# Kernel optimization log

Hardware: AMD Instinct MI355X
Metric: run time of the kernel (lower is better)

The kernel has to match this reference:

```python
import jax, jax.numpy as jnp
import numpy as np

BN_EPS = 1e-5
NUM_GRAPHS = 64


def setup_inputs() -> dict:
    key = jax.random.key(0)
    ks = jax.random.split(key, 10)
    N, F, H, E = 50000, 128, 256, 800000
    x = jax.random.normal(ks[0], (N, F), dtype=jnp.float32)
    edge_index = jax.random.randint(ks[1], (2, E), 0, N, dtype=jnp.int64)
    batch = jnp.sort(jax.random.randint(ks[2], (N,), 0, NUM_GRAPHS, dtype=jnp.int64))
    # Linear weights stored as [in, out]; y = z @ w + b (equivalent to torch Linear)
    w1_0 = jax.random.normal(ks[3], (F, H), dtype=jnp.float32) / np.sqrt(F)
    b1_0 = jnp.zeros((H,), jnp.float32)
    w2_0 = jax.random.normal(ks[4], (H, H), dtype=jnp.float32) / np.sqrt(H)
    b2_0 = jnp.zeros((H,), jnp.float32)
    g_0 = jnp.ones((H,), jnp.float32)
    be_0 = jnp.zeros((H,), jnp.float32)
    w1_r = jax.random.normal(ks[5], (3, H, H), dtype=jnp.float32) / np.sqrt(H)
    b1_r = jnp.zeros((3, H), jnp.float32)
    w2_r = jax.random.normal(ks[6], (3, H, H), dtype=jnp.float32) / np.sqrt(H)
    b2_r = jnp.zeros((3, H), jnp.float32)
    g_r = jnp.ones((3, H), jnp.float32)
    be_r = jnp.zeros((3, H), jnp.float32)
    return dict(x=x, edge_index=edge_index, batch=batch,
                w1_0=w1_0, b1_0=b1_0, w2_0=w2_0, b2_0=b2_0, g_0=g_0, be_0=be_0,
                w1_r=w1_r, b1_r=b1_r, w2_r=w2_r, b2_r=b2_r, g_r=g_r, be_r=be_r)


def _gin_layer(h, src, dst, n, w1, b1, w2, b2, g, be):
    # GINConv with eps=0: MLP(h_i + sum_{j->i} h_j), scatter-add over edges
    agg = jax.ops.segment_sum(h[src], dst, num_segments=n)  # [N, d]
    z = agg + h
    z = jnp.maximum(z @ w1 + b1, 0.0)
    z = z @ w2 + b2
    # BatchNorm1d over the node dimension (training-mode batch statistics)
    mu = jnp.mean(z, axis=0)
    var = jnp.var(z, axis=0)
    z = (z - mu) * jax.lax.rsqrt(var + BN_EPS) * g + be
    return jnp.maximum(z, 0.0)  # ReLU; dropout is identity in eval mode


def reference(x, edge_index, batch, w1_0, b1_0, w2_0, b2_0, g_0, be_0,
              w1_r, b1_r, w2_r, b2_r, g_r, be_r):
    src, dst = edge_index[0], edge_index[1]
    n = x.shape[0]
    h = _gin_layer(x, src, dst, n, w1_0, b1_0, w2_0, b2_0, g_0, be_0)
    for i in range(3):
        h = _gin_layer(h, src, dst, n, w1_r[i], b1_r[i], w2_r[i], b2_r[i], g_r[i], be_r[i])
    # global mean pool per graph id
    counts = jax.ops.segment_sum(jnp.ones((n,), h.dtype), batch, num_segments=NUM_GRAPHS)
    pooled = jax.ops.segment_sum(h, batch, num_segments=NUM_GRAPHS)
    return pooled / jnp.maximum(counts, 1.0)[:, None]
```

## Files before the change

### kernel.cpp

```cpp
#include <hip/hip_runtime.h>

typedef float  f32x4 __attribute__((ext_vector_type(4)));
typedef _Float16 half8 __attribute__((ext_vector_type(8)));

#define BN_EPS 1e-5f
#define NGRAPH 64

struct PrepArgs {
    const float* src[8];
    _Float16*    dst[8];
    int          K[8];
};

__global__ void prep_weights(PrepArgs a) {
    int m = blockIdx.y;
    int K = a.K[m];
    int total = K << 8;
    int idx = blockIdx.x * blockDim.x + threadIdx.x;
    if (idx >= total) return;
    int n = idx / K;
    int k = idx - n * K;
    a.dst[m][idx] = (_Float16)a.src[m][(size_t)k * 256 + n];
}

__global__ void cast_x(const float* __restrict__ x, _Float16* __restrict__ o, int total) {
    int i = (blockIdx.x * blockDim.x + threadIdx.x) << 3;
    if (i >= total) return;
    f32x4 a = *(const f32x4*)(x + i);
    f32x4 b = *(const f32x4*)(x + i + 4);
    half8 r;
#pragma unroll
    for (int k = 0; k < 4; ++k) { r[k] = (_Float16)a[k]; r[k + 4] = (_Float16)b[k]; }
    *(half8*)(o + i) = r;
}

__global__ void edge_count(const int* __restrict__ ei, int* __restrict__ cnt,
                           int* __restrict__ rank, int E) {
    int e = blockIdx.x * blockDim.x + threadIdx.x;
    if (e < E) rank[e] = atomicAdd(&cnt[ei[E + e]], 1);
}

__global__ void scan_p1(const int* __restrict__ cnt, int* __restrict__ part, int N) {
    __shared__ int lds[256];
    int idx = blockIdx.x * 256 + threadIdx.x;
    lds[threadIdx.x] = (idx < N) ? cnt[idx] : 0;
    __syncthreads();
    for (int d = 128; d > 0; d >>= 1) {
        if (threadIdx.x < d) lds[threadIdx.x] += lds[threadIdx.x + d];
        __syncthreads();
    }
    if (threadIdx.x == 0) part[blockIdx.x] = lds[0];
}

__global__ void scan_p2(int* __restrict__ part, int* __restrict__ off, int N, int nb) {
    __shared__ int lds[256];
    int t = threadIdx.x;
    int v = (t < nb) ? part[t] : 0;
    lds[t] = v;
    __syncthreads();
    for (int d = 1; d < 256; d <<= 1) {
        int a = (t >= d) ? lds[t - d] : 0;
        __syncthreads();
        lds[t] += a;
        __syncthreads();
    }
    if (t < nb) part[t] = lds[t] - v;
    if (t == nb - 1) off[N] = lds[t];
}

__global__ void scan_p3(const int* __restrict__ cnt, const int* __restrict__ part,
                        int* __restrict__ off, int N) {
    __shared__ int lds[256];
    int t = threadIdx.x;
    int idx = blockIdx.x * 256 + t;
    int v = (idx < N) ? cnt[idx] : 0;
    lds[t] = v;
    __syncthreads();
    for (int d = 1; d < 256; d <<= 1) {
        int a = (t >= d) ? lds[t - d] : 0;
        __syncthreads();
        lds[t] += a;
        __syncthreads();
    }
    if (idx < N) off[idx] = part[blockIdx.x] + lds[t] - v;
}

__global__ void edge_fill(const int* __restrict__ ei, const int* __restrict__ off,
                          const int* __restrict__ rank, int* __restrict__ csr_src, int E) {
    int e = blockIdx.x * blockDim.x + threadIdx.x;
    if (e >= E) return;
    csr_src[off[ei[E + e]] + rank[e]] = ei[e];
}

__global__ void gather0(const _Float16* __restrict__ x, const int* __restrict__ off,
                        const int* __restrict__ srcs, _Float16* __restrict__ out, int N) {
    int wid = (blockIdx.x << 2) + (threadIdx.x >> 6);
    if (wid >= N) return;
    int lane = threadIdx.x & 63;
    int q = lane >> 4;
    int fb = (lane & 15) << 3;
    const char* xb = (const char*)x;
    float acc[8] = {0.f, 0.f, 0.f, 0.f, 0.f, 0.f, 0.f, 0.f};
    int end = off[wid + 1];
    int e = off[wid] + q;
    unsigned fb2 = (unsigned)fb << 1;
    for (; e + 12 < end; e += 16) {
        half8 v0 = *(const half8*)(xb + (((unsigned)srcs[e] << 8) + fb2));
        half8 v1 = *(const half8*)(xb + (((unsigned)srcs[e + 4] << 8) + fb2));
        half8 v2 = *(const half8*)(xb + (((unsigned)srcs[e + 8] << 8) + fb2));
        half8 v3 = *(const half8*)(xb + (((unsigned)srcs[e + 12] << 8) + fb2));
#pragma unroll
        for (int k = 0; k < 8; ++k)
            acc[k] += ((float)v0[k] + (float)v1[k]) + ((float)v2[k] + (float)v3[k]);
    }
    for (; e + 4 < end; e += 8) {
        half8 v0 = *(const half8*)(xb + (((unsigned)srcs[e] << 8) + fb2));
        half8 v1 = *(const half8*)(xb + (((unsigned)srcs[e + 4] << 8) + fb2));
#pragma unroll
        for (int k = 0; k < 8; ++k) acc[k] += (float)v0[k] + (float)v1[k];
    }
    if (e < end) {
        half8 v0 = *(const half8*)(xb + (((unsigned)srcs[e] << 8) + fb2));
#pragma unroll
        for (int k = 0; k < 8; ++k) acc[k] += (float)v0[k];
    }
    if (q == 0) {
        half8 v = *(const half8*)(xb + (((unsigned)wid << 8) + fb2));
#pragma unroll
        for (int k = 0; k < 8; ++k) acc[k] += (float)v[k];
    }
#pragma unroll
    for (int k = 0; k < 8; ++k) {
        acc[k] += __shfl_xor(acc[k], 16);
        acc[k] += __shfl_xor(acc[k], 32);
    }
    if (q == 0) {
        half8 o;
#pragma unroll
        for (int k = 0; k < 8; ++k) o[k] = (_Float16)acc[k];
        *(half8*)(out + (size_t)wid * 128 + fb) = o;
    }
}

__global__ void gather_fused(const _Float16* __restrict__ z, const int* __restrict__ off,
                             const int* __restrict__ srcs, const float* __restrict__ stats,
                             const float* __restrict__ gam, const float* __restrict__ bet,
                             _Float16* __restrict__ out, int N, float invN) {
    int wid = (blockIdx.x << 2) + (threadIdx.x >> 6);
    if (wid >= N) return;
    int lane = threadIdx.x & 63;
    int hf = lane >> 5;
    int fb = (lane & 31) << 3;
    half8 sc8, tc8;
#pragma unroll
    for (int k = 0; k < 8; ++k) {
        float mu = stats[fb + k] * invN;
        float var = stats[256 + fb + k] * invN - mu * mu;
        float s = gam[fb + k] * rsqrtf(var + BN_EPS);
        sc8[k] = (_Float16)s;
        tc8[k] = (_Float16)(bet[fb + k] - mu * s);
    }
    const half8 zero8 = {0, 0, 0, 0, 0, 0, 0, 0};
    const char* zb = (const char*)z;
    unsigned fb2 = (unsigned)fb << 1;
    float acc[8] = {0.f, 0.f, 0.f, 0.f, 0.f, 0.f, 0.f, 0.f};
    int end = off[wid + 1];
    int e = off[wid] + hf;
    for (; e + 14 < end; e += 16) {
        half8 v0 = *(const half8*)(zb + (((unsigned)srcs[e] << 9) + fb2));
        half8 v1 = *(const half8*)(zb + (((unsigned)srcs[e + 2] << 9) + fb2));
        half8 v2 = *(const half8*)(zb + (((unsigned)srcs[e + 4] << 9) + fb2));
        half8 v3 = *(const half8*)(zb + (((unsigned)srcs[e + 6] << 9) + fb2));
        half8 v4 = *(const half8*)(zb + (((unsigned)srcs[e + 8] << 9) + fb2));
        half8 v5 = *(const half8*)(zb + (((unsigned)srcs[e + 10] << 9) + fb2));
        half8 v6 = *(const half8*)(zb + (((unsigned)srcs[e + 12] << 9) + fb2));
        half8 v7 = *(const half8*)(zb + (((unsigned)srcs[e + 14] << 9) + fb2));
        half8 r0 = __builtin_elementwise_max(v0 * sc8 + tc8, zero8);
        half8 r1 = __builtin_elementwise_max(v1 * sc8 + tc8, zero8);
        half8 r2 = __builtin_elementwise_max(v2 * sc8 + tc8, zero8);
        half8 r3 = __builtin_elementwise_max(v3 * sc8 + tc8, zero8);
        half8 r4 = __builtin_elementwise_max(v4 * sc8 + tc8, zero8);
        half8 r5 = __builtin_elementwise_max(v5 * sc8 + tc8, zero8);
        half8 r6 = __builtin_elementwise_max(v6 * sc8 + tc8, zero8);
        half8 r7 = __builtin_elementwise_max(v7 * sc8 + tc8, zero8);
#pragma unroll
        for (int k = 0; k < 8; ++k)
            acc[k] += (((float)r0[k] + (float)r1[k]) + ((float)r2[k] + (float)r3[k]))
                    + (((float)r4[k] + (float)r5[k]) + ((float)r6[k] + (float)r7[k]));
    }
    for (; e + 6 < end; e += 8) {
        half8 v0 = *(const half8*)(zb + (((unsigned)srcs[e] << 9) + fb2));
        half8 v1 = *(const half8*)(zb + (((unsigned)srcs[e + 2] << 9) + fb2));
        half8 v2 = *(const half8*)(zb + (((unsigned)srcs[e + 4] << 9) + fb2));
        half8 v3 = *(const half8*)(zb + (((unsigned)srcs[e + 6] << 9) + fb2));
        half8 r0 = __builtin_elementwise_max(v0 * sc8 + tc8, zero8);
        half8 r1 = __builtin_elementwise_max(v1 * sc8 + tc8, zero8);
        half8 r2 = __builtin_elementwise_max(v2 * sc8 + tc8, zero8);
        half8 r3 = __builtin_elementwise_max(v3 * sc8 + tc8, zero8);
#pragma unroll
        for (int k = 0; k < 8; ++k)
            acc[k] += ((float)r0[k] + (float)r1[k]) + ((float)r2[k] + (float)r3[k]);
    }
    for (; e < end; e += 2) {
        half8 v0 = *(const half8*)(zb + (((unsigned)srcs[e] << 9) + fb2));
        half8 r0 = __builtin_elementwise_max(v0 * sc8 + tc8, zero8);
#pragma unroll
        for (int k = 0; k < 8; ++k) acc[k] += (float)r0[k];
    }
    if (hf == 0) {
        half8 v = *(const half8*)(zb + (((unsigned)wid << 9) + fb2));
        half8 r = __builtin_elementwise_max(v * sc8 + tc8, zero8);
#pragma unroll
        for (int k = 0; k < 8; ++k) acc[k] += (float)r[k];
    }
#pragma unroll
    for (int k = 0; k < 8; ++k) acc[k] += __shfl_xor(acc[k], 32);
    if (hf == 0) {
        half8 o;
#pragma unroll
        for (int k = 0; k < 8; ++k) o[k] = (_Float16)acc[k];
        *(half8*)(out + (size_t)wid * 256 + fb) = o;
    }
}

template <int K, int WITH_STATS>
__global__ __launch_bounds__(512, 4) void gemm_kernel(
    const _Float16* __restrict__ A, const _Float16* __restrict__ BT,
    const float* __restrict__ bias, _Float16* __restrict__ Y,
    float* __restrict__ stats, int M) {
    extern __shared__ _Float16 blds[];
    float* sred = (float*)(blds + 17408);
    const int tid = threadIdx.x;
    const int lane = tid & 63, wave = tid >> 6;
    const int i = lane & 15, g = lane >> 4;
    const int rowbase = blockIdx.x * 128 + wave * 16;
    const int arow = min(rowbase + i, M - 1);

    half8 afrag[K / 32];
#pragma unroll
    for (int s = 0; s < K / 32; ++s)
        afrag[s] = *(const half8*)(A + (size_t)arow * K + s * 32 + g * 8);

    f32x4 acc[16];
#pragma unroll
    for (int t = 0; t < 16; ++t) acc[t] = (f32x4){0.f, 0.f, 0.f, 0.f};

    const int scol = tid >> 1;
    const int shalf = (tid & 1) * 32;
    const int ssw = (scol & 7) << 3;
    const int swi = (i & 7) << 3;

#pragma unroll
    for (int kc = 0; kc < K / 64; ++kc) {
        if (kc) __syncthreads();
        {
            const _Float16* src = BT + (size_t)scol * K + kc * 64 + shalf;
            _Float16* dst = blds + scol * 64;
#pragma unroll
            for (int c = 0; c < 32; c += 8)
                *(half8*)(dst + ((shalf + c) ^ ssw)) = *(const half8*)(src + c);
        }
        __syncthreads();
#pragma unroll
        for (int ks = 0; ks < 2; ++ks)
#pragma unroll
            for (int t = 0; t < 16; ++t) {
                half8 b = *(const half8*)(blds + (t * 16 + i) * 64 + ((ks * 32 + g * 8) ^ swi));
                acc[t] = __builtin_amdgcn_mfma_f32_16x16x32_f16(afrag[kc * 2 + ks], b, acc[t], 0, 0, 0);
            }
    }

    const int rg = g * 4;
    if (WITH_STATS) {
#pragma unroll
        for (int t = 0; t < 16; ++t) {
            int c = t * 16 + i;
            float bv = bias[c];
            float s1 = 0.f, s2 = 0.f;
#pragma unroll
            for (int j = 0; j < 4; ++j) {
                if (rowbase + rg + j < M) {
                    float v = acc[t][j] + bv;
                    s1 += v;
                    s2 += v * v;
                }
            }
            s1 += __shfl_xor(s1, 16); s1 += __shfl_xor(s1, 32);
            s2 += __shfl_xor(s2, 16); s2 += __shfl_xor(s2, 32);
            if (g == 0) {
                sred[wave * 256 + c] = s1;
                sred[2048 + wave * 256 + c] = s2;
            }
        }
    }
    __syncthreads();
    if (WITH_STATS) {
        int which = tid >> 8, c = tid & 255;
        float s = 0.f;
#pragma unroll
        for (int w = 0; w < 8; ++w) s += sred[which * 2048 + w * 256 + c];
        atomicAdd(&stats[which * 256 + c], s);
    }

    _Float16* ostage = blds;
#pragma unroll
    for (int ph = 0; ph < 2; ++ph) {
        if (ph) __syncthreads();
#pragma unroll
        for (int tt = 0; tt < 8; ++tt) {
            int t = ph * 8 + tt;
            int lc = tt * 16 + i;
            float bv = bias[t * 16 + i];
#pragma unroll
            for (int j = 0; j < 4; ++j) {
                float v = acc[t][j] + bv;
                if (WITH_STATS == 0) v = fmaxf(v, 0.f);
                ostage[(wave * 16 + rg + j) * 136 + lc] = (_Float16)v;
            }
        }
        __syncthreads();
#pragma unroll
        for (int k = 0; k < 4; ++k) {
            int ch = k * 512 + tid;
            int rl = ch >> 4, pc = (ch & 15) << 3;
            int r = blockIdx.x * 128 + rl;
            if (r < M)
                *(half8*)(Y + (size_t)r * 256 + ph * 128 + pc) =
                    *(const half8*)(ostage + rl * 136 + pc);
        }
    }
}

__global__ void graph_bounds(const int* __restrict__ batch, int* __restrict__ gstart, int N) {
    int t = threadIdx.x;
    if (t > NGRAPH) return;
    if (t == NGRAPH) { gstart[t] = N; return; }
    int lo = 0, hi = N;
    while (lo < hi) { int m = (lo + hi) >> 1; if (batch[m] < t) lo = m + 1; else hi = m; }
    gstart[t] = lo;
}

#define PCHUNK 256
__global__ void pool_stage1(const _Float16* __restrict__ z, const int* __restrict__ batch,
                            const int* __restrict__ gstart, const float* __restrict__ stats,
                            const float* __restrict__ gam, const float* __restrict__ bet,
                            float* __restrict__ acc, int N, float invN) {
    __shared__ float lds[8 * 512];
    int c0 = blockIdx.x * PCHUNK;
    int cend = min(c0 + PCHUNK, N);
    int tid = threadIdx.x;
    int rowlane = tid >> 5;
    int fb = (tid & 31) << 3;
    float sc[8], tc[8];
#pragma unroll
    for (int k = 0; k < 8; ++k) {
        float mu = stats[fb + k] * invN;
        float var = stats[256 + fb + k] * invN - mu * mu;
        float s = gam[fb + k] * rsqrtf(var + BN_EPS);
        sc[k] = s;
        tc[k] = bet[fb + k] - mu * s;
    }
    int segs = c0;
    while (segs < cend) {
        int g = batch[segs];
        int sege = min(gstart[g + 1], cend);
        float a[8] = {0.f, 0.f, 0.f, 0.f, 0.f, 0.f, 0.f, 0.f};
        for (int r = segs + rowlane; r < sege; r += 16) {
            half8 v = *(const half8*)(z + (size_t)r * 256 + fb);
#pragma unroll
            for (int k = 0; k < 8; ++k)
                a[k] += fmaxf(fmaf((float)v[k], sc[k], tc[k]), 0.f);
        }
#pragma unroll
        for (int k = 0; k < 8; ++k) lds[k * 512 + tid] = a[k];
        __syncthreads();
#pragma unroll
        for (int d = 8; d > 0; d >>= 1) {
            if (rowlane < d) {
#pragma unroll
                for (int k = 0; k < 8; ++k)
                    lds[k * 512 + tid] += lds[k * 512 + tid + d * 32];
            }
            __syncthreads();
        }
        if (rowlane == 0) {
#pragma unroll
            for (int k = 0; k < 8; ++k)
                atomicAdd(&acc[g * 256 + fb + k], lds[k * 512 + tid]);
        }
        __syncthreads();
        segs = sege;
    }
}

__global__ void pool_finalize(const float* __restrict__ acc, const int* __restrict__ gstart,
                              float* __restrict__ out) {
    int i = blockIdx.x * 256 + threadIdx.x;
    int g = i >> 8;
    int c = gstart[g + 1] - gstart[g];
    out[i] = acc[i] / (float)(c > 0 ? c : 1);
}

extern "C" void kernel_launch(void* const* d_in, const int* in_sizes, int n_in,
                              void* d_out, int out_size, void* d_ws, size_t ws_size,
                              hipStream_t stream) {
    const float* x    = (const float*)d_in[0];
    const int*   ei   = (const int*)d_in[1];
    const int*   batch= (const int*)d_in[2];
    const float* w1_0 = (const float*)d_in[3];
    const float* b1_0 = (const float*)d_in[4];
    const float* w2_0 = (const float*)d_in[5];
    const float* b2_0 = (const float*)d_in[6];
    const float* g_0  = (const float*)d_in[7];
    const float* be_0 = (const float*)d_in[8];
    const float* w1_r = (const float*)d_in[9];
    const float* b1_r = (const float*)d_in[10];
    const float* w2_r = (const float*)d_in[11];
    const float* b2_r = (const float*)d_in[12];
    const float* g_r  = (const float*)d_in[13];
    const float* be_r = (const float*)d_in[14];

    const int N = in_sizes[0] / 128;
    const int E = in_sizes[1] / 2;

    char* p = (char*)d_ws;
    auto alloc = [&](size_t bytes) { char* r = p; p += (bytes + 255) & ~(size_t)255; return r; };
    float*    stats   = (float*)alloc(4 * 512 * sizeof(float));
    int*      part    = (int*)alloc(256 * sizeof(int));
    int*      off     = (int*)alloc((size_t)(N + 1) * sizeof(int));
    int*      cnt     = (int*)alloc((size_t)N * sizeof(int));
    int*      gstart  = (int*)alloc(65 * sizeof(int));
    float*    accp    = (float*)alloc(NGRAPH * 256 * sizeof(float));
    int*      rank    = (int*)alloc((size_t)E * sizeof(int));
    int*      csr_src = (int*)alloc((size_t)E * sizeof(int));
    _Float16* wT      = (_Float16*)alloc((size_t)491520 * sizeof(_Float16));
    _Float16* x16     = (_Float16*)alloc((size_t)N * 128 * sizeof(_Float16));
    _Float16* zin     = (_Float16*)alloc((size_t)N * 256 * sizeof(_Float16));
    _Float16* y       = (_Float16*)alloc((size_t)N * 256 * sizeof(_Float16));
    _Float16* z       = (_Float16*)alloc((size_t)N * 256 * sizeof(_Float16));

    hipMemsetAsync(stats, 0, 4 * 512 * sizeof(float), stream);
    hipMemsetAsync(cnt, 0, (size_t)N * sizeof(int), stream);
    hipMemsetAsync(accp, 0, NGRAPH * 256 * sizeof(float), stream);

    PrepArgs pa;
    pa.src[0] = w1_0;  pa.dst[0] = wT;           pa.K[0] = 128;
    pa.src[1] = w2_0;  pa.dst[1] = wT + 32768;   pa.K[1] = 256;
    for (int i = 0; i < 3; ++i) {
        pa.src[2 + i] = w1_r + (size_t)i * 65536; pa.dst[2 + i] = wT + 98304 + (size_t)i * 65536; pa.K[2 + i] = 256;
        pa.src[5 + i] = w2_r + (size_t)i * 65536; pa.dst[5 + i] = wT + 294912 + (size_t)i * 65536; pa.K[5 + i] = 256;
    }
    prep_weights<<<dim3(256, 8), 256, 0, stream>>>(pa);
    cast_x<<<(N * 128 / 8 + 255) / 256, 256, 0, stream>>>(x, x16, N * 128);

    const int eb = (E + 255) / 256;
    const int nb = (N + 255) / 256;
    edge_count<<<eb, 256, 0, stream>>>(ei, cnt, rank, E);
    scan_p1<<<nb, 256, 0, stream>>>(cnt, part, N);
    scan_p2<<<1, 256, 0, stream>>>(part, off, N, nb);
    scan_p3<<<nb, 256, 0, stream>>>(cnt, part, off, N);
    edge_fill<<<eb, 256, 0, stream>>>(ei, off, rank, csr_src, E);
    graph_bounds<<<1, 128, 0, stream>>>(batch, gstart, N);

    const int gwb = (N + 3) / 4;
    const int gemmg = (N + 127) / 128;
    const int ldsb = 51200;
    const float invN = 1.0f / (float)N;

    gather0<<<gwb, 256, 0, stream>>>(x16, off, csr_src, zin, N);
    gemm_kernel<128, 0><<<gemmg, 512, ldsb, stream>>>(zin, wT, b1_0, y, nullptr, N);
    gemm_kernel<256, 1><<<gemmg, 512, ldsb, stream>>>(y, wT + 32768, b2_0, z, stats, N);

    const float* cur_stats = stats;
    const float* cur_g = g_0;
    const float* cur_be = be_0;
    for (int i = 0; i < 3; ++i) {
        gather_fused<<<gwb, 256, 0, stream>>>(z, off, csr_src, cur_stats, cur_g, cur_be, zin, N, invN);
        gemm_kernel<256, 0><<<gemmg, 512, ldsb, stream>>>(
            zin, wT + 98304 + (size_t)i * 65536, b1_r + i * 256, y, nullptr, N);
        gemm_kernel<256, 1><<<gemmg, 512, ldsb, stream>>>(
            y, wT + 294912 + (size_t)i * 65536, b2_r + i * 256, z, stats + (i + 1) * 512, N);
        cur_stats = stats + (i + 1) * 512;
        cur_g = g_r + i * 256;
        cur_be = be_r + i * 256;
    }

    pool_stage1<<<(N + PCHUNK - 1) / PCHUNK, 512, 0, stream>>>(
        z, batch, gstart, cur_stats, cur_g, cur_be, accp, N, invN);
    pool_finalize<<<NGRAPH, 256, 0, stream>>>(accp, gstart, (float*)d_out);
}
```

Measured before the change: 476.0 us.

## Store node features in 32-column slabs so each gather block reads a compact feature slice

Node features are now stored in a slab layout: feature-major chunks of 32 columns, each chunk laid out [N,32]. The cast, the GEMM input and output paths, and pooling are all changed to read or write this layout. A new gather kernel gives each block a single slab, so the random neighbour gathers touch a smaller working set that should stay resident in cache, at the cost of re-reading CSR indices once per slab and issuing 8-byte loads instead of 16-byte loads. The BN scale and shift are computed once per layer in a tiny kernel instead of by every wave.

New measurement: 752.1 us. 58.0% more time.

```diff
diff --git a/kernel.cpp b/kernel.cpp
--- a/kernel.cpp
+++ b/kernel.cpp
@@ -2,6 +2,7 @@
 
 typedef float  f32x4 __attribute__((ext_vector_type(4)));
 typedef _Float16 half8 __attribute__((ext_vector_type(8)));
+typedef _Float16 half4 __attribute__((ext_vector_type(4)));
 
 #define BN_EPS 1e-5f
 #define NGRAPH 64
@@ -23,15 +24,16 @@
     a.dst[m][idx] = (_Float16)a.src[m][(size_t)k * 256 + n];
 }
 
-__global__ void cast_x(const float* __restrict__ x, _Float16* __restrict__ o, int total) {
+__global__ void cast_x_slab(const float* __restrict__ x, _Float16* __restrict__ o, int N) {
     int i = (blockIdx.x * blockDim.x + threadIdx.x) << 3;
-    if (i >= total) return;
+    if (i >= N * 128) return;
+    int n = i >> 7, f = i & 127;
     f32x4 a = *(const f32x4*)(x + i);
     f32x4 b = *(const f32x4*)(x + i + 4);
     half8 r;
 #pragma unroll
     for (int k = 0; k < 4; ++k) { r[k] = (_Float16)a[k]; r[k + 4] = (_Float16)b[k]; }
-    *(half8*)(o + i) = r;
+    *(half8*)(o + (size_t)(f >> 5) * N * 32 + (size_t)n * 32 + (f & 31)) = r;
 }
 
 __global__ void edge_count(const int* __restrict__ ei, int* __restrict__ cnt,
@@ -92,138 +94,69 @@
     csr_src[off[ei[E + e]] + rank[e]] = ei[e];
 }
 
-__global__ void gather0(const _Float16* __restrict__ x, const int* __restrict__ off,
-                        const int* __restrict__ srcs, _Float16* __restrict__ out, int N) {
-    int wid = (blockIdx.x << 2) + (threadIdx.x >> 6);
+__global__ void bn_coef(const float* __restrict__ stats, const float* __restrict__ gam,
+                        const float* __restrict__ bet, _Float16* __restrict__ c16,
+                        float* __restrict__ c32, float invN) {
+    int c = threadIdx.x;
+    float mu = stats[c] * invN;
+    float var = stats[256 + c] * invN - mu * mu;
+    float s = gam[c] * rsqrtf(var + BN_EPS);
+    float t = bet[c] - mu * s;
+    c16[c] = (_Float16)s; c16[256 + c] = (_Float16)t;
+    c32[c] = s; c32[256 + c] = t;
+}
+
+template <int AFFINE>
+__global__ void gather_slab(const _Float16* __restrict__ in, const int* __restrict__ off,
+                            const int* __restrict__ srcs, const _Float16* __restrict__ coef,
+                            _Float16* __restrict__ out, int N, int slabmask_log2) {
+    int slab = blockIdx.x & ((1 << slabmask_log2) - 1);
+    int wid = (blockIdx.x >> slabmask_log2) * 4 + (threadIdx.x >> 6);
     if (wid >= N) return;
     int lane = threadIdx.x & 63;
-    int q = lane >> 4;
-    int fb = (lane & 15) << 3;
-    const char* xb = (const char*)x;
-    float acc[8] = {0.f, 0.f, 0.f, 0.f, 0.f, 0.f, 0.f, 0.f};
-    int end = off[wid + 1];
-    int e = off[wid] + q;
-    unsigned fb2 = (unsigned)fb << 1;
-    for (; e + 12 < end; e += 16) {
-        half8 v0 = *(const half8*)(xb + (((unsigned)srcs[e] << 8) + fb2));
-        half8 v1 = *(const half8*)(xb + (((unsigned)srcs[e + 4] << 8) + fb2));
-        half8 v2 = *(const half8*)(xb + (((unsigned)srcs[e + 8] << 8) + fb2));
-        half8 v3 = *(const half8*)(xb + (((unsigned)srcs[e + 12] << 8) + fb2));
-#pragma unroll
-        for (int k = 0; k < 8; ++k)
-            acc[k] += ((float)v0[k] + (float)v1[k]) + ((float)v2[k] + (float)v3[k]);
-    }
-    for (; e + 4 < end; e += 8) {
-        half8 v0 = *(const half8*)(xb + (((unsigned)srcs[e] << 8) + fb2));
-        half8 v1 = *(const half8*)(xb + (((unsigned)srcs[e + 4] << 8) + fb2));
-#pragma unroll
-        for (int k = 0; k < 8; ++k) acc[k] += (float)v0[k] + (float)v1[k];
-    }
-    if (e < end) {
-        half8 v0 = *(const half8*)(xb + (((unsigned)srcs[e] << 8) + fb2));
-#pragma unroll
-        for (int k = 0; k < 8; ++k) acc[k] += (float)v0[k];
-    }
-    if (q == 0) {
-        half8 v = *(const half8*)(xb + (((unsigned)wid << 8) + fb2));
-#pragma unroll
-        for (int k = 0; k < 8; ++k) acc[k] += (float)v[k];
-    }
-#pragma unroll
-    for (int k = 0; k < 8; ++k) {
+    int grp = lane >> 3;
+    int fl = (lane & 7) << 2;
+    size_t sbase = (size_t)slab * N * 32;
+    const _Float16* zsl = in + sbase;
+    half4 sc4, tc4;
+    const half4 zero4 = {0, 0, 0, 0};
+    if (AFFINE) {
+        sc4 = *(const half4*)(coef + slab * 32 + fl);
+        tc4 = *(const half4*)(coef + 256 + slab * 32 + fl);
+    }
+    float acc[4] = {0.f, 0.f, 0.f, 0.f};
+    int beg = off[wid], end = off[wid + 1];
+    for (int e = beg; e < end; e += 8) {
+        int edge = e + grp;
+        if (edge < end) {
+            int src = srcs[edge];
+            half4 v = *(const half4*)(zsl + (size_t)src * 32 + fl);
+            if (AFFINE) v = __builtin_elementwise_max(v * sc4 + tc4, zero4);
+#pragma unroll
+            for (int k = 0; k < 4; ++k) acc[k] += (float)v[k];
+        }
+    }
+    if (grp == 0) {
+        half4 v = *(const half4*)(zsl + (size_t)wid * 32 + fl);
+        if (AFFINE) v = __builtin_elementwise_max(v * sc4 + tc4, zero4);
+#pragma unroll
+        for (int k = 0; k < 4; ++k) acc[k] += (float)v[k];
+    }
+#pragma unroll
+    for (int k = 0; k < 4; ++k) {
+        acc[k] += __shfl_xor(acc[k], 8);
         acc[k] += __shfl_xor(acc[k], 16);
         acc[k] += __shfl_xor(acc[k], 32);
     }
-    if (q == 0) {
-        half8 o;
-#pragma unroll
-        for (int k = 0; k < 8; ++k) o[k] = (_Float16)acc[k];
-        *(half8*)(out + (size_t)wid * 128 + fb) = o;
-    }
-}
-
-__global__ void gather_fused(const _Float16* __restrict__ z, const int* __restrict__ off,
-                             const int* __restrict__ srcs, const float* __restrict__ stats,
-                             const float* __restrict__ gam, const float* __restrict__ bet,
-                             _Float16* __restrict__ out, int N, float invN) {
-    int wid = (blockIdx.x << 2) + (threadIdx.x >> 6);
-    if (wid >= N) return;
-    int lane = threadIdx.x & 63;
-    int hf = lane >> 5;
-    int fb = (lane & 31) << 3;
-    half8 sc8, tc8;
-#pragma unroll
-    for (int k = 0; k < 8; ++k) {
-        float mu = stats[fb + k] * invN;
-        float var = stats[256 + fb + k] * invN - mu * mu;
-        float s = gam[fb + k] * rsqrtf(var + BN_EPS);
-        sc8[k] = (_Float16)s;
-        tc8[k] = (_Float16)(bet[fb + k] - mu * s);
-    }
-    const half8 zero8 = {0, 0, 0, 0, 0, 0, 0, 0};
-    const char* zb = (const char*)z;
-    unsigned fb2 = (unsigned)fb << 1;
-    float acc[8] = {0.f, 0.f, 0.f, 0.f, 0.f, 0.f, 0.f, 0.f};
-    int end = off[wid + 1];
-    int e = off[wid] + hf;
-    for (; e + 14 < end; e += 16) {
-        half8 v0 = *(const half8*)(zb + (((unsigned)srcs[e] << 9) + fb2));
-        half8 v1 = *(const half8*)(zb + (((unsigned)srcs[e + 2] << 9) + fb2));
-        half8 v2 = *(const half8*)(zb + (((unsigned)srcs[e + 4] << 9) + fb2));
-        half8 v3 = *(const half8*)(zb + (((unsigned)srcs[e + 6] << 9) + fb2));
-        half8 v4 = *(const half8*)(zb + (((unsigned)srcs[e + 8] << 9) + fb2));
-        half8 v5 = *(const half8*)(zb + (((unsigned)srcs[e + 10] << 9) + fb2));
-        half8 v6 = *(const half8*)(zb + (((unsigned)srcs[e + 12] << 9) + fb2));
-        half8 v7 = *(const half8*)(zb + (((unsigned)srcs[e + 14] << 9) + fb2));
-        half8 r0 = __builtin_elementwise_max(v0 * sc8 + tc8, zero8);
-        half8 r1 = __builtin_elementwise_max(v1 * sc8 + tc8, zero8);
-        half8 r2 = __builtin_elementwise_max(v2 * sc8 + tc8, zero8);
-        half8 r3 = __builtin_elementwise_max(v3 * sc8 + tc8, zero8);
-        half8 r4 = __builtin_elementwise_max(v4 * sc8 + tc8, zero8);
-        half8 r5 = __builtin_elementwise_max(v5 * sc8 + tc8, zero8);
-        half8 r6 = __builtin_elementwise_max(v6 * sc8 + tc8, zero8);
-        half8 r7 = __builtin_elementwise_max(v7 * sc8 + tc8, zero8);
-#pragma unroll
-        for (int k = 0; k < 8; ++k)
-            acc[k] += (((float)r0[k] + (float)r1[k]) + ((float)r2[k] + (float)r3[k]))
-                    + (((float)r4[k] + (float)r5[k]) + ((float)r6[k] + (float)r7[k]));
-    }
-    for (; e + 6 < end; e += 8) {
-        half8 v0 = *(const half8*)(zb + (((unsigned)srcs[e] << 9) + fb2));
-        half8 v1 = *(const half8*)(zb + (((unsigned)srcs[e + 2] << 9) + fb2));
-        half8 v2 = *(const half8*)(zb + (((unsigned)srcs[e + 4] << 9) + fb2));
-        half8 v3 = *(const half8*)(zb + (((unsigned)srcs[e + 6] << 9) + fb2));
-        half8 r0 = __builtin_elementwise_max(v0 * sc8 + tc8, zero8);
-        half8 r1 = __builtin_elementwise_max(v1 * sc8 + tc8, zero8);
-        half8 r2 = __builtin_elementwise_max(v2 * sc8 + tc8, zero8);
-        half8 r3 = __builtin_elementwise_max(v3 * sc8 + tc8, zero8);
-#pragma unroll
-        for (int k = 0; k < 8; ++k)
-            acc[k] += ((float)r0[k] + (float)r1[k]) + ((float)r2[k] + (float)r3[k]);
-    }
-    for (; e < end; e += 2) {
-        half8 v0 = *(const half8*)(zb + (((unsigned)srcs[e] << 9) + fb2));
-        half8 r0 = __builtin_elementwise_max(v0 * sc8 + tc8, zero8);
-#pragma unroll
-        for (int k = 0; k < 8; ++k) acc[k] += (float)r0[k];
-    }
-    if (hf == 0) {
-        half8 v = *(const half8*)(zb + (((unsigned)wid << 9) + fb2));
-        half8 r = __builtin_elementwise_max(v * sc8 + tc8, zero8);
-#pragma unroll
-        for (int k = 0; k < 8; ++k) acc[k] += (float)r[k];
-    }
-#pragma unroll
-    for (int k = 0; k < 8; ++k) acc[k] += __shfl_xor(acc[k], 32);
-    if (hf == 0) {
-        half8 o;
-#pragma unroll
-        for (int k = 0; k < 8; ++k) o[k] = (_Float16)acc[k];
-        *(half8*)(out + (size_t)wid * 256 + fb) = o;
-    }
-}
-
-template <int K, int WITH_STATS>
+    if (grp == 0) {
+        half4 o;
+#pragma unroll
+        for (int k = 0; k < 4; ++k) o[k] = (_Float16)acc[k];
+        *(half4*)(out + sbase + (size_t)wid * 32 + fl) = o;
+    }
+}
+
+template <int K, int WITH_STATS, int IN_SLAB, int OUT_SLAB>
 __global__ __launch_bounds__(512, 4) void gemm_kernel(
     const _Float16* __restrict__ A, const _Float16* __restrict__ BT,
     const float* __restrict__ bias, _Float16* __restrict__ Y,
@@ -239,7 +172,9 @@
     half8 afrag[K / 32];
 #pragma unroll
     for (int s = 0; s < K / 32; ++s)
-        afrag[s] = *(const half8*)(A + (size_t)arow * K + s * 32 + g * 8);
+        afrag[s] = IN_SLAB
+            ? *(const half8*)(A + (size_t)s * M * 32 + (size_t)arow * 32 + g * 8)
+            : *(const half8*)(A + (size_t)arow * K + s * 32 + g * 8);
 
     f32x4 acc[16];
 #pragma unroll
@@ -319,14 +254,25 @@
             }
         }
         __syncthreads();
-#pragma unroll
-        for (int k = 0; k < 4; ++k) {
-            int ch = k * 512 + tid;
-            int rl = ch >> 4, pc = (ch & 15) << 3;
+        if (OUT_SLAB) {
+            int rl = tid >> 2, pp = (tid & 3) << 3;
             int r = blockIdx.x * 128 + rl;
-            if (r < M)
-                *(half8*)(Y + (size_t)r * 256 + ph * 128 + pc) =
-                    *(const half8*)(ostage + rl * 136 + pc);
+#pragma unroll
+            for (int k = 0; k < 4; ++k) {
+                if (r < M)
+                    *(half8*)(Y + (size_t)(ph * 4 + k) * M * 32 + (size_t)r * 32 + pp) =
+                        *(const half8*)(ostage + rl * 136 + k * 32 + pp);
+            }
+        } else {
+#pragma unroll
+            for (int k = 0; k < 4; ++k) {
+                int ch = k * 512 + tid;
+                int rl = ch >> 4, pc = (ch & 15) << 3;
+                int r = blockIdx.x * 128 + rl;
+                if (r < M)
+                    *(half8*)(Y + (size_t)r * 256 + ph * 128 + pc) =
+                        *(const half8*)(ostage + rl * 136 + pc);
+            }
         }
     }
 }
@@ -342,31 +288,26 @@
 
 #define PCHUNK 256
 __global__ void pool_stage1(const _Float16* __restrict__ z, const int* __restrict__ batch,
-                            const int* __restrict__ gstart, const float* __restrict__ stats,
-                            const float* __restrict__ gam, const float* __restrict__ bet,
-                            float* __restrict__ acc, int N, float invN) {
+                            const int* __restrict__ gstart, const float* __restrict__ c32,
+                            float* __restrict__ acc, int N) {
     __shared__ float lds[8 * 512];
     int c0 = blockIdx.x * PCHUNK;
     int cend = min(c0 + PCHUNK, N);
     int tid = threadIdx.x;
     int rowlane = tid >> 5;
     int fb = (tid & 31) << 3;
+    size_t sbase = (size_t)(fb >> 5) * N * 32;
+    int fo = fb & 31;
     float sc[8], tc[8];
 #pragma unroll
-    for (int k = 0; k < 8; ++k) {
-        float mu = stats[fb + k] * invN;
-        float var = stats[256 + fb + k] * invN - mu * mu;
-        float s = gam[fb + k] * rsqrtf(var + BN_EPS);
-        sc[k] = s;
-        tc[k] = bet[fb + k] - mu * s;
-    }
+    for (int k = 0; k < 8; ++k) { sc[k] = c32[fb + k]; tc[k] = c32[256 + fb + k]; }
     int segs = c0;
     while (segs < cend) {
         int g = batch[segs];
         int sege = min(gstart[g + 1], cend);
         float a[8] = {0.f, 0.f, 0.f, 0.f, 0.f, 0.f, 0.f, 0.f};
         for (int r = segs + rowlane; r < sege; r += 16) {
-            half8 v = *(const half8*)(z + (size_t)r * 256 + fb);
+            half8 v = *(const half8*)(z + sbase + (size_t)r * 32 + fo);
 #pragma unroll
             for (int k = 0; k < 8; ++k)
                 a[k] += fmaxf(fmaf((float)v[k], sc[k], tc[k]), 0.f);
@@ -426,6 +367,8 @@
     char* p = (char*)d_ws;
     auto alloc = [&](size_t bytes) { char* r = p; p += (bytes + 255) & ~(size_t)255; return r; };
     float*    stats   = (float*)alloc(4 * 512 * sizeof(float));
+    _Float16* coef16  = (_Float16*)alloc(512 * sizeof(_Float16));
+    float*    coef32  = (float*)alloc(512 * sizeof(float));
     int*      part    = (int*)alloc(256 * sizeof(int));
     int*      off     = (int*)alloc((size_t)(N + 1) * sizeof(int));
     int*      cnt     = (int*)alloc((size_t)N * sizeof(int));
@@ -451,7 +394,7 @@
         pa.src[5 + i] = w2_r + (size_t)i * 65536; pa.dst[5 + i] = wT + 294912 + (size_t)i * 65536; pa.K[5 + i] = 256;
     }
     prep_weights<<<dim3(256, 8), 256, 0, stream>>>(pa);
-    cast_x<<<(N * 128 / 8 + 255) / 256, 256, 0, stream>>>(x, x16, N * 128);
+    cast_x_slab<<<(N * 128 / 8 + 255) / 256, 256, 0, stream>>>(x, x16, N);
 
     const int eb = (E + 255) / 256;
     const int nb = (N + 255) / 256;
@@ -462,30 +405,27 @@
     edge_fill<<<eb, 256, 0, stream>>>(ei, off, rank, csr_src, E);
     graph_bounds<<<1, 128, 0, stream>>>(batch, gstart, N);
 
-    const int gwb = (N + 3) / 4;
+    const int nch = (N + 3) / 4;
     const int gemmg = (N + 127) / 128;
     const int ldsb = 51200;
     const float invN = 1.0f / (float)N;
 
-    gather0<<<gwb, 256, 0, stream>>>(x16, off, csr_src, zin, N);
-    gemm_kernel<128, 0><<<gemmg, 512, ldsb, stream>>>(zin, wT, b1_0, y, nullptr, N);
-    gemm_kernel<256, 1><<<gemmg, 512, ldsb, stream>>>(y, wT + 32768, b2_0, z, stats, N);
-
-    const float* cur_stats = stats;
-    const float* cur_g = g_0;
-    const float* cur_be = be_0;
+    gather_slab<0><<<nch * 4, 256, 0, stream>>>(x16, off, csr_src, nullptr, zin, N, 2);
+    gemm_kernel<128, 0, 1, 0><<<gemmg, 512, ldsb, stream>>>(zin, wT, b1_0, y, nullptr, N);
+    gemm_kernel<256, 1, 0, 1><<<gemmg, 512, ldsb, stream>>>(y, wT + 32768, b2_0, z, stats, N);
+    bn_coef<<<1, 256, 0, stream>>>(stats, g_0, be_0, coef16, coef32, invN);
+
     for (int i = 0; i < 3; ++i) {
-        gather_fused<<<gwb, 256, 0, stream>>>(z, off, csr_src, cur_stats, cur_g, cur_be, zin, N, invN);
-        gemm_kernel<256, 0><<<gemmg, 512, ldsb, stream>>>(
+        gather_slab<1><<<nch * 8, 256, 0, stream>>>(z, off, csr_src, coef16, zin, N, 3);
+        gemm_kernel<256, 0, 1, 0><<<gemmg, 512, ldsb, stream>>>(
             zin, wT + 98304 + (size_t)i * 65536, b1_r + i * 256, y, nullptr, N);
-        gemm_kernel<256, 1><<<gemmg, 512, ldsb, stream>>>(
+        gemm_kernel<256, 1, 0, 1><<<gemmg, 512, ldsb, stream>>>(
             y, wT + 294912 + (size_t)i * 65536, b2_r + i * 256, z, stats + (i + 1) * 512, N);
-        cur_stats = stats + (i + 1) * 512;
-        cur_g = g_r + i * 256;
-        cur_be = be_r + i * 256;
+        bn_coef<<<1, 256, 0, stream>>>(stats + (i + 1) * 512, g_r + i * 256, be_r + i * 256,
+                                       coef16, coef32, invN);
     }
 
     pool_stage1<<<(N + PCHUNK - 1) / PCHUNK, 512, 0, stream>>>(
-        z, batch, gstart, cur_stats, cur_g, cur_be, accp, N, invN);
+        z, batch, gstart, coef32, accp, N);
     pool_finalize<<<NGRAPH, 256, 0, stream>>>(accp, gstart, (float*)d_out);
 }
```

## Precompute BN coefficients in tiny kernel and shrink gather unrolling with half-precision pair sums

Applied to the files above, without the earlier changes.

Adds a bn_coef kernel that computes BatchNorm scale and shift once per layer in fp16 and fp32. Gather and pool kernels now load these coefficients directly instead of recomputing them per wave from stats, gamma and beta. The deepest unrolled edge loops in both gathers are removed, and pairs of loaded rows are summed in fp16 before converting to fp32. This cuts per-wave setup work, register pressure and convert/add instructions, but adds four small kernel launches, exposes fewer loads in flight per wave, and loses some accuracy from the fp16 partial sums.

Result: no change. 475.6 us (-0.1%).

```diff
diff --git a/kernel.cpp b/kernel.cpp
--- a/kernel.cpp
+++ b/kernel.cpp
@@ -92,6 +92,18 @@
     csr_src[off[ei[E + e]] + rank[e]] = ei[e];
 }
 
+__global__ void bn_coef(const float* __restrict__ stats, const float* __restrict__ gam,
+                        const float* __restrict__ bet, _Float16* __restrict__ c16,
+                        float* __restrict__ c32, float invN) {
+    int c = threadIdx.x;
+    float mu = stats[c] * invN;
+    float var = stats[256 + c] * invN - mu * mu;
+    float s = gam[c] * rsqrtf(var + BN_EPS);
+    float t = bet[c] - mu * s;
+    c16[c] = (_Float16)s; c16[256 + c] = (_Float16)t;
+    c32[c] = s; c32[256 + c] = t;
+}
+
 __global__ void gather0(const _Float16* __restrict__ x, const int* __restrict__ off,
                         const int* __restrict__ srcs, _Float16* __restrict__ out, int N) {
     int wid = (blockIdx.x << 2) + (threadIdx.x >> 6);
@@ -100,24 +112,16 @@
     int q = lane >> 4;
     int fb = (lane & 15) << 3;
     const char* xb = (const char*)x;
+    unsigned fb2 = (unsigned)fb << 1;
     float acc[8] = {0.f, 0.f, 0.f, 0.f, 0.f, 0.f, 0.f, 0.f};
     int end = off[wid + 1];
     int e = off[wid] + q;
-    unsigned fb2 = (unsigned)fb << 1;
-    for (; e + 12 < end; e += 16) {
-        half8 v0 = *(const half8*)(xb + (((unsigned)srcs[e] << 8) + fb2));
-        half8 v1 = *(const half8*)(xb + (((unsigned)srcs[e + 4] << 8) + fb2));
-        half8 v2 = *(const half8*)(xb + (((unsigned)srcs[e + 8] << 8) + fb2));
-        half8 v3 = *(const half8*)(xb + (((unsigned)srcs[e + 12] << 8) + fb2));
-#pragma unroll
-        for (int k = 0; k < 8; ++k)
-            acc[k] += ((float)v0[k] + (float)v1[k]) + ((float)v2[k] + (float)v3[k]);
-    }
     for (; e + 4 < end; e += 8) {
         half8 v0 = *(const half8*)(xb + (((unsigned)srcs[e] << 8) + fb2));
         half8 v1 = *(const half8*)(xb + (((unsigned)srcs[e + 4] << 8) + fb2));
-#pragma unroll
-        for (int k = 0; k < 8; ++k) acc[k] += (float)v0[k] + (float)v1[k];
+        half8 p = v0 + v1;
+#pragma unroll
+        for (int k = 0; k < 8; ++k) acc[k] += (float)p[k];
     }
     if (e < end) {
         half8 v0 = *(const half8*)(xb + (((unsigned)srcs[e] << 8) + fb2));
@@ -143,51 +147,21 @@
 }
 
 __global__ void gather_fused(const _Float16* __restrict__ z, const int* __restrict__ off,
-                             const int* __restrict__ srcs, const float* __restrict__ stats,
-                             const float* __restrict__ gam, const float* __restrict__ bet,
-                             _Float16* __restrict__ out, int N, float invN) {
+                             const int* __restrict__ srcs, const _Float16* __restrict__ coef,
+                             _Float16* __restrict__ out, int N) {
     int wid = (blockIdx.x << 2) + (threadIdx.x >> 6);
     if (wid >= N) return;
     int lane = threadIdx.x & 63;
     int hf = lane >> 5;
     int fb = (lane & 31) << 3;
-    half8 sc8, tc8;
-#pragma unroll
-    for (int k = 0; k < 8; ++k) {
-        float mu = stats[fb + k] * invN;
-        float var = stats[256 + fb + k] * invN - mu * mu;
-        float s = gam[fb + k] * rsqrtf(var + BN_EPS);
-        sc8[k] = (_Float16)s;
-        tc8[k] = (_Float16)(bet[fb + k] - mu * s);
-    }
+    half8 sc8 = *(const half8*)(coef + fb);
+    half8 tc8 = *(const half8*)(coef + 256 + fb);
     const half8 zero8 = {0, 0, 0, 0, 0, 0, 0, 0};
     const char* zb = (const char*)z;
     unsigned fb2 = (unsigned)fb << 1;
     float acc[8] = {0.f, 0.f, 0.f, 0.f, 0.f, 0.f, 0.f, 0.f};
     int end = off[wid + 1];
     int e = off[wid] + hf;
-    for (; e + 14 < end; e += 16) {
-        half8 v0 = *(const half8*)(zb + (((unsigned)srcs[e] << 9) + fb2));
-        half8 v1 = *(const half8*)(zb + (((unsigned)srcs[e + 2] << 9) + fb2));
-        half8 v2 = *(const half8*)(zb + (((unsigned)srcs[e + 4] << 9) + fb2));
-        half8 v3 = *(const half8*)(zb + (((unsigned)srcs[e + 6] << 9) + fb2));
-        half8 v4 = *(const half8*)(zb + (((unsigned)srcs[e + 8] << 9) + fb2));
-        half8 v5 = *(const half8*)(zb + (((unsigned)srcs[e + 10] << 9) + fb2));
-        half8 v6 = *(const half8*)(zb + (((unsigned)srcs[e + 12] << 9) + fb2));
-        half8 v7 = *(const half8*)(zb + (((unsigned)srcs[e + 14] << 9) + fb2));
-        half8 r0 = __builtin_elementwise_max(v0 * sc8 + tc8, zero8);
-        half8 r1 = __builtin_elementwise_max(v1 * sc8 + tc8, zero8);
-        half8 r2 = __builtin_elementwise_max(v2 * sc8 + tc8, zero8);
-        half8 r3 = __builtin_elementwise_max(v3 * sc8 + tc8, zero8);
-        half8 r4 = __builtin_elementwise_max(v4 * sc8 + tc8, zero8);
-        half8 r5 = __builtin_elementwise_max(v5 * sc8 + tc8, zero8);
-        half8 r6 = __builtin_elementwise_max(v6 * sc8 + tc8, zero8);
-        half8 r7 = __builtin_elementwise_max(v7 * sc8 + tc8, zero8);
-#pragma unroll
-        for (int k = 0; k < 8; ++k)
-            acc[k] += (((float)r0[k] + (float)r1[k]) + ((float)r2[k] + (float)r3[k]))
-                    + (((float)r4[k] + (float)r5[k]) + ((float)r6[k] + (float)r7[k]));
-    }
     for (; e + 6 < end; e += 8) {
         half8 v0 = *(const half8*)(zb + (((unsigned)srcs[e] << 9) + fb2));
         half8 v1 = *(const half8*)(zb + (((unsigned)srcs[e + 2] << 9) + fb2));
@@ -197,9 +171,11 @@
         half8 r1 = __builtin_elementwise_max(v1 * sc8 + tc8, zero8);
         half8 r2 = __builtin_elementwise_max(v2 * sc8 + tc8, zero8);
         half8 r3 = __builtin_elementwise_max(v3 * sc8 + tc8, zero8);
+        half8 p01 = r0 + r1;
+        half8 p23 = r2 + r3;
 #pragma unroll
         for (int k = 0; k < 8; ++k)
-            acc[k] += ((float)r0[k] + (float)r1[k]) + ((float)r2[k] + (float)r3[k]);
+            acc[k] += (float)p01[k] + (float)p23[k];
     }
     for (; e < end; e += 2) {
         half8 v0 = *(const half8*)(zb + (((unsigned)srcs[e] << 9) + fb2));
@@ -342,9 +318,8 @@
 
 #define PCHUNK 256
 __global__ void pool_stage1(const _Float16* __restrict__ z, const int* __restrict__ batch,
-                            const int* __restrict__ gstart, const float* __restrict__ stats,
-                            const float* __restrict__ gam, const float* __restrict__ bet,
-                            float* __restrict__ acc, int N, float invN) {
+                            const int* __restrict__ gstart, const float* __restrict__ c32,
+                            float* __restrict__ acc, int N) {
     __shared__ float lds[8 * 512];
     int c0 = blockIdx.x * PCHUNK;
     int cend = min(c0 + PCHUNK, N);
@@ -353,13 +328,7 @@
     int fb = (tid & 31) << 3;
     float sc[8], tc[8];
 #pragma unroll
-    for (int k = 0; k < 8; ++k) {
-        float mu = stats[fb + k] * invN;
-        float var = stats[256 + fb + k] * invN - mu * mu;
-        float s = gam[fb + k] * rsqrtf(var + BN_EPS);
-        sc[k] = s;
-        tc[k] = bet[fb + k] - mu * s;
-    }
+    for (int k = 0; k < 8; ++k) { sc[k] = c32[fb + k]; tc[k] = c32[256 + fb + k]; }
     int segs = c0;
     while (segs < cend) {
         int g = batch[segs];
@@ -426,6 +395,8 @@
     char* p = (char*)d_ws;
     auto alloc = [&](size_t bytes) { char* r = p; p += (bytes + 255) & ~(size_t)255; return r; };
     float*    stats   = (float*)alloc(4 * 512 * sizeof(float));
+    _Float16* coef16  = (_Float16*)alloc(512 * sizeof(_Float16));
+    float*    coef32  = (float*)alloc(512 * sizeof(float));
     int*      part    = (int*)alloc(256 * sizeof(int));
     int*      off     = (int*)alloc((size_t)(N + 1) * sizeof(int));
     int*      cnt     = (int*)alloc((size_t)N * sizeof(int));
@@ -470,22 +441,19 @@
     gather0<<<gwb, 256, 0, stream>>>(x16, off, csr_src, zin, N);
     gemm_kernel<128, 0><<<gemmg, 512, ldsb, stream>>>(zin, wT, b1_0, y, nullptr, N);
     gemm_kernel<256, 1><<<gemmg, 512, ldsb, stream>>>(y, wT + 32768, b2_0, z, stats, N);
-
-    const float* cur_stats = stats;
-    const float* cur_g = g_0;
-    const float* cur_be = be_0;
+    bn_coef<<<1, 256, 0, stream>>>(stats, g_0, be_0, coef16, coef32, invN);
+
     for (int i = 0; i < 3; ++i) {
-        gather_fused<<<gwb, 256, 0, stream>>>(z, off, csr_src, cur_stats, cur_g, cur_be, zin, N, invN);
+        gather_fused<<<gwb, 256, 0, stream>>>(z, off, csr_src, coef16, zin, N);
         gemm_kernel<256, 0><<<gemmg, 512, ldsb, stream>>>(
             zin, wT + 98304 + (size_t)i * 65536, b1_r + i * 256, y, nullptr, N);
         gemm_kernel<256, 1><<<gemmg, 512, ldsb, stream>>>(
             y, wT + 294912 + (size_t)i * 65536, b2_r + i * 256, z, stats + (i + 1) * 512, N);
-        cur_stats = stats + (i + 1) * 512;
-        cur_g = g_r + i * 256;
-        cur_be = be_r + i * 256;
+        bn_coef<<<1, 256, 0, stream>>>(stats + (i + 1) * 512, g_r + i * 256, be_r + i * 256,
+                                       coef16, coef32, invN);
     }
 
     pool_stage1<<<(N + PCHUNK - 1) / PCHUNK, 512, 0, stream>>>(
-        z, batch, gstart, cur_stats, cur_g, cur_be, accp, N, invN);
+        z, batch, gstart, coef32, accp, N);
     pool_finalize<<<NGRAPH, 256, 0, stream>>>(accp, gstart, (float*)d_out);
 }
```
